# Optimization experiments

Hardware: AMD Instinct MI355X
Metric: run time of the kernel (lower is better)

## Reference

```python
import jax, jax.numpy as jnp
import numpy as np

N = 50000
E = 800000
NUM_KINDS = 100
D_NODE = 64
D_EDGE = 4
D_MSG = 64
L = 3
D_IN = 2 * D_NODE + D_EDGE  # 132


def setup_inputs() -> dict:
    key = jax.random.key(0)
    ks = jax.random.split(key, 20)

    def w(k, shape, fan_in):
        bound = 1.0 / np.sqrt(fan_in)
        return jax.random.uniform(k, shape, jnp.float32, -bound, bound)

    inp = {
        "edge_index": jax.random.randint(ks[0], (2, E), 0, N),
        "node_kind_ids": jax.random.randint(ks[1], (N,), 0, NUM_KINDS),
        "edge_attr": jax.random.normal(ks[2], (E, D_EDGE), jnp.float32),
        # learned params
        "emb": jax.random.normal(ks[3], (NUM_KINDS, D_NODE), jnp.float32),
        # stacked per-layer message MLP params [L, ...]
        "msg_w1": w(ks[4], (L, D_MSG, D_IN), D_IN),
        "msg_b1": w(ks[5], (L, D_MSG), D_IN),
        "msg_w2": w(ks[6], (L, D_MSG, D_MSG), D_MSG),
        "msg_b2": w(ks[7], (L, D_MSG), D_MSG),
        # stacked per-layer GRUCell params (torch layout: [3*d_node, d_in])
        "gru_wih": w(ks[8], (L, 3 * D_NODE, D_MSG), D_NODE),
        "gru_whh": w(ks[9], (L, 3 * D_NODE, D_NODE), D_NODE),
        "gru_bih": w(ks[10], (L, 3 * D_NODE), D_NODE),
        "gru_bhh": w(ks[11], (L, 3 * D_NODE), D_NODE),
        # edge head: Linear(132,64) -> SiLU -> Linear(64,1)
        "head_w1": w(ks[12], (64, D_IN), D_IN),
        "head_b1": w(ks[13], (64,), D_IN),
        "head_w2": w(ks[14], (1, 64), 64),
        "head_b2": w(ks[15], (1,), 64),
    }
    return inp


def reference(edge_index, node_kind_ids, edge_attr, emb,
              msg_w1, msg_b1, msg_w2, msg_b2,
              gru_wih, gru_whh, gru_bih, gru_bhh,
              head_w1, head_b1, head_w2, head_b2):
    src, dst = edge_index[0], edge_index[1]
    h = emb[node_kind_ids]  # [N, d_node]
    n_nodes = h.shape[0]
    for l in range(L):
        x = jnp.concatenate([h[src], h[dst], edge_attr], axis=1)  # [E, 132]
        m = jax.nn.silu(x @ msg_w1[l].T + msg_b1[l]) @ msg_w2[l].T + msg_b2[l]  # [E, d_msg]
        agg = jax.ops.segment_sum(m, dst, num_segments=n_nodes)  # [N, d_msg]
        # torch GRUCell math
        gi = agg @ gru_wih[l].T + gru_bih[l]  # [N, 3*d_node]
        gh = h @ gru_whh[l].T + gru_bhh[l]
        ir, iz, inn = jnp.split(gi, 3, axis=1)
        hr, hz, hn = jnp.split(gh, 3, axis=1)
        r = jax.nn.sigmoid(ir + hr)
        z = jax.nn.sigmoid(iz + hz)
        n = jnp.tanh(inn + r * hn)
        h = (1.0 - z) * n + z * h
    x = jnp.concatenate([h[src], h[dst], edge_attr], axis=1)  # [E, 132]
    logits = (jax.nn.silu(x @ head_w1.T + head_b1) @ head_w2.T + head_b2)[:, 0]
    return jax.nn.sigmoid(logits)  # [E]
```

## Files before the change

### kernel.cpp

```cpp
#include <hip/hip_runtime.h>
#include <hip/hip_bf16.h>


typedef __attribute__((ext_vector_type(8))) short bf16x8;
typedef __attribute__((ext_vector_type(4))) float f32x4;
#define MFMA16(a, b, c) __builtin_amdgcn_mfma_f32_16x16x32_bf16(a, b, c, 0, 0, 0)

#define CHUNK 128
#define XSTRIDE 272
#define MSTRIDE 264
#define HSTRIDE 144
#define SLABSZ 8704
#define HIDSZ  4608

#define WRZST 264
#define WNST  136

__device__ __forceinline__ float fast_sig(float x) { return 1.f / (1.f + __expf(-x)); }
__device__ __forceinline__ float fast_tanh(float x) {
    float ax = fabsf(x);
    float t = __expf(-2.f * ax);
    return copysignf((1.f - t) / (1.f + t), x);
}
__device__ __forceinline__ ushort f2bf(float f) {
    unsigned u = __float_as_uint(f);
    unsigned r = u + 0x7FFF + ((u >> 16) & 1);
    return (ushort)(r >> 16);
}

__global__ void prep_kernel(const float* __restrict__ msg_w1,
                            const float* __restrict__ msg_w2,
                            const float* __restrict__ gru_wih,
                            const float* __restrict__ gru_whh,
                            const float* __restrict__ head_w1,
                            const float* __restrict__ head_w2,
                            ushort* __restrict__ Wb1, ushort* __restrict__ Wb2,
                            ushort* __restrict__ Wh1, ushort* __restrict__ Wh2b,
                            ushort* __restrict__ Wrz, ushort* __restrict__ Wni,
                            ushort* __restrict__ Wnh) {
    int t = blockIdx.x * 256 + threadIdx.x;
    if (t < 30720) {
        int l = t / 10240, r = t % 10240, j = r / 160, k = r % 160;
        Wb1[t] = (k < 132) ? f2bf(msg_w1[l * 8448 + j * 132 + k]) : 0;
        return;
    }
    t -= 30720;
    if (t < 12288) {
        Wb2[t] = f2bf(msg_w2[t]);
        return;
    }
    t -= 12288;
    if (t < 10240) {
        int j = t / 160, k = t % 160;
        Wh1[t] = (k < 132) ? f2bf(head_w1[j * 132 + k]) : 0;
        return;
    }
    t -= 10240;
    if (t < 1024) {
        int j = t >> 6, k = t & 63;
        Wh2b[t] = (j == 0) ? f2bf(head_w2[k]) : 0;
        return;
    }
    t -= 1024;
    if (t < 49152) {
        int l = t / 16384, r = t % 16384, n = r >> 7, k = r & 127;
        float v = (k < 64) ? gru_wih[l * 12288 + n * 64 + k]
                           : gru_whh[l * 12288 + n * 64 + (k - 64)];
        Wrz[t] = f2bf(v);
        return;
    }
    t -= 49152;
    if (t < 12288) {
        int l = t / 4096, r = t % 4096, j = r >> 6, k = r & 63;
        Wni[t] = f2bf(gru_wih[l * 12288 + (128 + j) * 64 + k]);
        return;
    }
    t -= 12288;
    if (t < 12288) {
        int l = t / 4096, r = t % 4096, j = r >> 6, k = r & 63;
        Wnh[t] = f2bf(gru_whh[l * 12288 + (128 + j) * 64 + k]);
    }
}

__global__ void embed_kernel(float* __restrict__ h, ushort* __restrict__ hb,
                             const float* __restrict__ emb,
                             const int* __restrict__ kinds, int N) {
    int t = blockIdx.x * 256 + threadIdx.x;
    if (t >= N * 64) return;
    int node = t >> 6, d = t & 63;
    float v = emb[kinds[node] * 64 + d];
    h[t] = v;
    hb[t] = f2bf(v);
}

__global__ void hist_kernel(const int* __restrict__ dst, int* __restrict__ deg, int E) {
    int e = blockIdx.x * 256 + threadIdx.x;
    if (e < E) atomicAdd(&deg[dst[e]], 1);
}

__global__ void scan_kernel(const int* __restrict__ deg, int* __restrict__ cursor, int N) {
    __shared__ int sums[1024];
    int tid = threadIdx.x;
    int chunk = (N + 1023) >> 10;
    int lo = tid * chunk, hi = min(lo + chunk, N);
    int s = 0;
    for (int i = lo; i < hi; i++) s += deg[i];
    sums[tid] = s;
    __syncthreads();
    for (int off = 1; off < 1024; off <<= 1) {
        int v = (tid >= off) ? sums[tid - off] : 0;
        __syncthreads();
        sums[tid] += v;
        __syncthreads();
    }
    int run = (tid > 0) ? sums[tid - 1] : 0;
    for (int i = lo; i < hi; i++) {
        cursor[i] = run;
        run += deg[i];
    }
}

__global__ void scatter_kernel(const int* __restrict__ src, const int* __restrict__ dst,
                               const float* __restrict__ ea, int* __restrict__ cursor,
                               int* __restrict__ src_s, int* __restrict__ dst_s,
                               ushort* __restrict__ ea_sb, int E) {
    int e = blockIdx.x * 256 + threadIdx.x;
    if (e >= E) return;
    int d = dst[e];
    int p = atomicAdd(&cursor[d], 1);
    src_s[p] = src[e];
    dst_s[p] = d;
    float4 e4 = ((const float4*)ea)[e];
    ushort4 eb;
    eb.x = f2bf(e4.x); eb.y = f2bf(e4.y); eb.z = f2bf(e4.z); eb.w = f2bf(e4.w);
    ((ushort4*)ea_sb)[p] = eb;
}

__global__ __launch_bounds__(256) void edge_msg_mfma(
    const ushort* __restrict__ hb, const int* __restrict__ src_s,
    const int* __restrict__ dst_s, const ushort* __restrict__ ea_sb,
    const ushort* __restrict__ Wb1l, const ushort* __restrict__ Wb2l,
    const float* __restrict__ b1, const float* __restrict__ b2,
    float* __restrict__ agg, int E, int nchunks) {
    __shared__ char lds[4 * SLABSZ + 4 * HIDSZ];
    int tid = threadIdx.x;
    int w = tid >> 6, lane = tid & 63;
    int quad = lane >> 4, nrow = lane & 15;
    char* slab = lds + w * SLABSZ;
    char* hidb = lds + 4 * SLABSZ + w * HIDSZ;

    bf16x8 wf1[4][4], wfea[4], wf2[4][2];
    float b1v[4], b2v[4];
#pragma unroll
    for (int nt = 0; nt < 4; nt++) {
        int n = nt * 16 + nrow;
#pragma unroll
        for (int ks = 0; ks < 4; ks++)
            wf1[nt][ks] = *(const bf16x8*)(Wb1l + n * 160 + ks * 32 + quad * 8);
        wfea[nt] = *(const bf16x8*)(Wb1l + n * 160 + 128 + quad * 8);
#pragma unroll
        for (int ks = 0; ks < 2; ks++)
            wf2[nt][ks] = *(const bf16x8*)(Wb2l + n * 64 + ks * 32 + quad * 8);
        b1v[nt] = b1[n];
        b2v[nt] = b2[n];
    }

    for (int chunk = blockIdx.x; chunk < nchunks; chunk += gridDim.x) {
        int ebase = chunk * CHUNK;
        {
            int el = tid >> 1, half = tid & 1;
            int r = el & 31;
            int ec = min(ebase + el, E - 1);
            int node = half ? dst_s[ec] : src_s[ec];
            const float4* hrow = (const float4*)(hb + (size_t)node * 64);
            float4* xw = (float4*)(slab + r * XSTRIDE + half * 128);
#pragma unroll
            for (int i = 0; i < 8; i++) xw[i] = hrow[i];
        }
        bf16x8 ea0 = {0, 0, 0, 0, 0, 0, 0, 0};
        bf16x8 ea1 = {0, 0, 0, 0, 0, 0, 0, 0};
        if (quad == 0) {
            int ec0 = min(ebase + w * 32 + nrow, E - 1);
            int ec1 = min(ebase + w * 32 + 16 + nrow, E - 1);
            *(uint2*)&ea0 = *(const uint2*)(ea_sb + (size_t)ec0 * 4);
            *(uint2*)&ea1 = *(const uint2*)(ea_sb + (size_t)ec1 * 4);
        }
        f32x4 acc1[2][4];
#pragma unroll
        for (int mt = 0; mt < 2; mt++)
#pragma unroll
            for (int nt = 0; nt < 4; nt++) {
                f32x4 v;
                v[0] = v[1] = v[2] = v[3] = b1v[nt];
                acc1[mt][nt] = v;
            }
#pragma unroll
        for (int ks = 0; ks < 4; ks++) {
            bf16x8 a0 = *(const bf16x8*)(slab + nrow * XSTRIDE + ks * 64 + quad * 16);
            bf16x8 a1 = *(const bf16x8*)(slab + (16 + nrow) * XSTRIDE + ks * 64 + quad * 16);
#pragma unroll
            for (int nt = 0; nt < 4; nt++) {
                acc1[0][nt] = MFMA16(a0, wf1[nt][ks], acc1[0][nt]);
                acc1[1][nt] = MFMA16(a1, wf1[nt][ks], acc1[1][nt]);
            }
        }
#pragma unroll
        for (int nt = 0; nt < 4; nt++) {
            acc1[0][nt] = MFMA16(ea0, wfea[nt], acc1[0][nt]);
            acc1[1][nt] = MFMA16(ea1, wfea[nt], acc1[1][nt]);
        }
#pragma unroll
        for (int mt = 0; mt < 2; mt++)
#pragma unroll
            for (int nt = 0; nt < 4; nt++)
#pragma unroll
                for (int rg = 0; rg < 4; rg++) {
                    float v = acc1[mt][nt][rg];
                    v = v * fast_sig(v);
                    int rm = mt * 16 + quad * 4 + rg;
                    *(ushort*)(hidb + rm * HSTRIDE + (nt * 16 + nrow) * 2) = f2bf(v);
                }
        f32x4 acc2[2][4];
#pragma unroll
        for (int mt = 0; mt < 2; mt++)
#pragma unroll
            for (int nt = 0; nt < 4; nt++) {
                f32x4 v;
                v[0] = v[1] = v[2] = v[3] = b2v[nt];
                acc2[mt][nt] = v;
            }
#pragma unroll
        for (int ks = 0; ks < 2; ks++) {
            bf16x8 a0 = *(const bf16x8*)(hidb + nrow * HSTRIDE + ks * 64 + quad * 16);
            bf16x8 a1 = *(const bf16x8*)(hidb + (16 + nrow) * HSTRIDE + ks * 64 + quad * 16);
#pragma unroll
            for (int nt = 0; nt < 4; nt++) {
                acc2[0][nt] = MFMA16(a0, wf2[nt][ks], acc2[0][nt]);
                acc2[1][nt] = MFMA16(a1, wf2[nt][ks], acc2[1][nt]);
            }
        }
#pragma unroll
        for (int mt = 0; mt < 2; mt++)
#pragma unroll
            for (int nt = 0; nt < 4; nt++)
#pragma unroll
                for (int rg = 0; rg < 4; rg++) {
                    int rm = mt * 16 + quad * 4 + rg;
                    *(float*)(slab + rm * MSTRIDE + (nt * 16 + nrow) * 4) = acc2[mt][nt][rg];
                }
        {
            int e32 = ebase + w * 32;
            int dmy = dst_s[min(e32 + (lane & 31), E - 1)];
            int limit = min(32, E - e32);
            int nx = __shfl_down(dmy, 1);
            bool tl = ((lane & 31) == 31) || (dmy != nx);
            unsigned long long tm = __ballot(tl);
            float run = 0.f;
#pragma unroll
            for (int i = 0; i < 32; i++) {
                if (i < limit) {
                    run += *(const float*)(slab + i * MSTRIDE + lane * 4);
                    if (((tm >> i) & 1ull) || (i + 1 == limit)) {
                        int di = __shfl(dmy, i);
                        unsafeAtomicAdd(&agg[(size_t)di * 64 + lane], run);
                        run = 0.f;
                    }
                }
            }
        }
    }
}

__global__ __launch_bounds__(256) void head_mfma(
    const ushort* __restrict__ hb, const int* __restrict__ src,
    const int* __restrict__ dst, const float* __restrict__ ea,
    const ushort* __restrict__ Wh1, const ushort* __restrict__ Wh2b,
    const float* __restrict__ hb1, const float* __restrict__ hb2p,
    float* __restrict__ out, int E, int nchunks) {
    __shared__ char lds[4 * SLABSZ + 4 * HIDSZ];
    int tid = threadIdx.x;
    int w = tid >> 6, lane = tid & 63;
    int quad = lane >> 4, nrow = lane & 15;
    char* slab = lds + w * SLABSZ;
    char* hidb = lds + 4 * SLABSZ + w * HIDSZ;

    bf16x8 wf1[4][4], wfea[4], wh2[2];
    float b1v[4];
#pragma unroll
    for (int nt = 0; nt < 4; nt++) {
        int n = nt * 16 + nrow;
#pragma unroll
        for (int ks = 0; ks < 4; ks++)
            wf1[nt][ks] = *(const bf16x8*)(Wh1 + n * 160 + ks * 32 + quad * 8);
        wfea[nt] = *(const bf16x8*)(Wh1 + n * 160 + 128 + quad * 8);
        b1v[nt] = hb1[n];
    }
#pragma unroll
    for (int ks = 0; ks < 2; ks++)
        wh2[ks] = *(const bf16x8*)(Wh2b + nrow * 64 + ks * 32 + quad * 8);
    float hb2 = hb2p[0];

    for (int chunk = blockIdx.x; chunk < nchunks; chunk += gridDim.x) {
        int ebase = chunk * CHUNK;
        {
            int el = tid >> 1, half = tid & 1;
            int r = el & 31;
            int ec = min(ebase + el, E - 1);
            int node = half ? dst[ec] : src[ec];
            const float4* hrow = (const float4*)(hb + (size_t)node * 64);
            float4* xw = (float4*)(slab + r * XSTRIDE + half * 128);
#pragma unroll
            for (int i = 0; i < 8; i++) xw[i] = hrow[i];
        }
        bf16x8 ea0 = {0, 0, 0, 0, 0, 0, 0, 0};
        bf16x8 ea1 = {0, 0, 0, 0, 0, 0, 0, 0};
        if (quad == 0) {
            int ec0 = min(ebase + w * 32 + nrow, E - 1);
            int ec1 = min(ebase + w * 32 + 16 + nrow, E - 1);
            float4 e0 = ((const float4*)ea)[ec0];
            float4 e1 = ((const float4*)ea)[ec1];
            ushort4 u0, u1;
            u0.x = f2bf(e0.x); u0.y = f2bf(e0.y); u0.z = f2bf(e0.z); u0.w = f2bf(e0.w);
            u1.x = f2bf(e1.x); u1.y = f2bf(e1.y); u1.z = f2bf(e1.z); u1.w = f2bf(e1.w);
            *(ushort4*)&ea0 = u0;
            *(ushort4*)&ea1 = u1;
        }
        f32x4 acc1[2][4];
#pragma unroll
        for (int mt = 0; mt < 2; mt++)
#pragma unroll
            for (int nt = 0; nt < 4; nt++) {
                f32x4 v;
                v[0] = v[1] = v[2] = v[3] = b1v[nt];
                acc1[mt][nt] = v;
            }
#pragma unroll
        for (int ks = 0; ks < 4; ks++) {
            bf16x8 a0 = *(const bf16x8*)(slab + nrow * XSTRIDE + ks * 64 + quad * 16);
            bf16x8 a1 = *(const bf16x8*)(slab + (16 + nrow) * XSTRIDE + ks * 64 + quad * 16);
#pragma unroll
            for (int nt = 0; nt < 4; nt++) {
                acc1[0][nt] = MFMA16(a0, wf1[nt][ks], acc1[0][nt]);
                acc1[1][nt] = MFMA16(a1, wf1[nt][ks], acc1[1][nt]);
            }
        }
#pragma unroll
        for (int nt = 0; nt < 4; nt++) {
            acc1[0][nt] = MFMA16(ea0, wfea[nt], acc1[0][nt]);
            acc1[1][nt] = MFMA16(ea1, wfea[nt], acc1[1][nt]);
        }
#pragma unroll
        for (int mt = 0; mt < 2; mt++)
#pragma unroll
            for (int nt = 0; nt < 4; nt++)
#pragma unroll
                for (int rg = 0; rg < 4; rg++) {
                    float v = acc1[mt][nt][rg];
                    v = v * fast_sig(v);
                    int rm = mt * 16 + quad * 4 + rg;
                    *(ushort*)(hidb + rm * HSTRIDE + (nt * 16 + nrow) * 2) = f2bf(v);
                }
        f32x4 acc3[2];
#pragma unroll
        for (int mt = 0; mt < 2; mt++) {
            f32x4 v;
            v[0] = v[1] = v[2] = v[3] = 0.f;
            acc3[mt] = v;
        }
#pragma unroll
        for (int ks = 0; ks < 2; ks++) {
            bf16x8 a0 = *(const bf16x8*)(hidb + nrow * HSTRIDE + ks * 64 + quad * 16);
            bf16x8 a1 = *(const bf16x8*)(hidb + (16 + nrow) * HSTRIDE + ks * 64 + quad * 16);
            acc3[0] = MFMA16(a0, wh2[ks], acc3[0]);
            acc3[1] = MFMA16(a1, wh2[ks], acc3[1]);
        }
        if (nrow == 0) {
#pragma unroll
            for (int mt = 0; mt < 2; mt++)
#pragma unroll
                for (int rg = 0; rg < 4; rg++) {
                    int e = ebase + w * 32 + mt * 16 + quad * 4 + rg;
                    if (e < E) out[e] = fast_sig(acc3[mt][rg] + hb2);
                }
        }
    }
}

__device__ __forceinline__ bf16x8 aggfrag(const float* __restrict__ row, int off) {
    float4 f0 = *(const float4*)(row + off);
    float4 f1 = *(const float4*)(row + off + 4);
    bf16x8 r;
    r[0] = (short)f2bf(f0.x); r[1] = (short)f2bf(f0.y);
    r[2] = (short)f2bf(f0.z); r[3] = (short)f2bf(f0.w);
    r[4] = (short)f2bf(f1.x); r[5] = (short)f2bf(f1.y);
    r[6] = (short)f2bf(f1.z); r[7] = (short)f2bf(f1.w);
    return r;
}

__global__ __launch_bounds__(256) void gru_mfma(
    float* __restrict__ h, ushort* __restrict__ hb, float* __restrict__ agg,
    const ushort* __restrict__ Wrzg, const ushort* __restrict__ Wnig,
    const ushort* __restrict__ Wnhg,
    const float* __restrict__ bih, const float* __restrict__ bhh, int N) {
    __shared__ char lds[128 * WRZST + 2 * 64 * WNST];
    int tid = threadIdx.x, w = tid >> 6, lane = tid & 63;
    int quad = lane >> 4, nrow = lane & 15;
    char* wrz = lds;
    char* wni = lds + 128 * WRZST;
    char* wnh = wni + 64 * WNST;

    {
        int r = tid >> 1, half = tid & 1;
        const uint4* g = (const uint4*)(Wrzg + r * 128 + half * 64);
        uint4* d = (uint4*)(wrz + r * WRZST + half * 128);
#pragma unroll
        for (int i = 0; i < 8; i++) d[i] = g[i];
        if (tid < 128) {
            const uint4* g2 = (const uint4*)(Wnig + (tid >> 1) * 64 + (tid & 1) * 32);
            uint4* d2 = (uint4*)(wni + (tid >> 1) * WNST + (tid & 1) * 64);
#pragma unroll
            for (int i = 0; i < 4; i++) d2[i] = g2[i];
        } else {
            int t2 = tid - 128;
            const uint4* g2 = (const uint4*)(Wnhg + (t2 >> 1) * 64 + (t2 & 1) * 32);
            uint4* d2 = (uint4*)(wnh + (t2 >> 1) * WNST + (t2 & 1) * 64);
#pragma unroll
            for (int i = 0; i < 4; i++) d2[i] = g2[i];
        }
    }
    __syncthreads();

    int nb0 = blockIdx.x * 128 + w * 32;
    if (nb0 >= N) return;

    float brz[8], bi[4], bhv[4];
#pragma unroll
    for (int nt = 0; nt < 8; nt++) brz[nt] = bih[nt * 16 + nrow] + bhh[nt * 16 + nrow];
#pragma unroll
    for (int nt = 0; nt < 4; nt++) {
        bi[nt] = bih[128 + nt * 16 + nrow];
        bhv[nt] = bhh[128 + nt * 16 + nrow];
    }

    int n0 = min(nb0 + nrow, N - 1);
    int n1 = min(nb0 + 16 + nrow, N - 1);
    const float* ag0 = agg + (size_t)n0 * 64;
    const float* ag1 = agg + (size_t)n1 * 64;
    const ushort* hb0 = hb + (size_t)n0 * 64;
    const ushort* hb1 = hb + (size_t)n1 * 64;

    f32x4 accrz[2][8], acci[2][4], acch[2][4];
#pragma unroll
    for (int nt = 0; nt < 8; nt++) {
        f32x4 v; v[0] = v[1] = v[2] = v[3] = brz[nt];
        accrz[0][nt] = v; accrz[1][nt] = v;
    }
#pragma unroll
    for (int nt = 0; nt < 4; nt++) {
        f32x4 vi; vi[0] = vi[1] = vi[2] = vi[3] = bi[nt];
        acci[0][nt] = vi; acci[1][nt] = vi;
        f32x4 vh; vh[0] = vh[1] = vh[2] = vh[3] = bhv[nt];
        acch[0][nt] = vh; acch[1][nt] = vh;
    }

#pragma unroll
    for (int ks = 0; ks < 4; ks++) {
        bf16x8 a0, a1;
        if (ks < 2) {
            a0 = aggfrag(ag0, ks * 32 + quad * 8);
            a1 = aggfrag(ag1, ks * 32 + quad * 8);
        } else {
            a0 = *(const bf16x8*)(hb0 + (ks - 2) * 32 + quad * 8);
            a1 = *(const bf16x8*)(hb1 + (ks - 2) * 32 + quad * 8);
        }
#pragma unroll
        for (int nt = 0; nt < 8; nt++) {
            bf16x8 b = *(const bf16x8*)(wrz + (nt * 16 + nrow) * WRZST + ks * 64 + quad * 16);
            accrz[0][nt] = MFMA16(a0, b, accrz[0][nt]);
            accrz[1][nt] = MFMA16(a1, b, accrz[1][nt]);
        }
        if (ks < 2) {
#pragma unroll
            for (int nt = 0; nt < 4; nt++) {
                bf16x8 b = *(const bf16x8*)(wni + (nt * 16 + nrow) * WNST + ks * 64 + quad * 16);
                acci[0][nt] = MFMA16(a0, b, acci[0][nt]);
                acci[1][nt] = MFMA16(a1, b, acci[1][nt]);
            }
        } else {
#pragma unroll
            for (int nt = 0; nt < 4; nt++) {
                bf16x8 b = *(const bf16x8*)(wnh + (nt * 16 + nrow) * WNST + (ks - 2) * 64 + quad * 16);
                acch[0][nt] = MFMA16(a0, b, acch[0][nt]);
                acch[1][nt] = MFMA16(a1, b, acch[1][nt]);
            }
        }
    }

#pragma unroll
    for (int mt = 0; mt < 2; mt++)
#pragma unroll
        for (int nt = 0; nt < 4; nt++)
#pragma unroll
            for (int rg = 0; rg < 4; rg++) {
                int node = nb0 + mt * 16 + quad * 4 + rg;
                if (node < N) {
                    int col = nt * 16 + nrow;
                    float r = fast_sig(accrz[mt][nt][rg]);
                    float z = fast_sig(accrz[mt][nt + 4][rg]);
                    float nn = fast_tanh(acci[mt][nt][rg] + r * acch[mt][nt][rg]);
                    size_t idx = (size_t)node * 64 + col;
                    float ho = h[idx];
                    float hnew = (1.f - z) * nn + z * ho;
                    h[idx] = hnew;
                    hb[idx] = f2bf(hnew);
                }
            }

    {
        float4 z4 = {0.f, 0.f, 0.f, 0.f};
        if (nb0 + nrow < N) {
            float* a = agg + (size_t)(nb0 + nrow) * 64;
            *(float4*)(a + quad * 8) = z4;
            *(float4*)(a + quad * 8 + 4) = z4;
            *(float4*)(a + 32 + quad * 8) = z4;
            *(float4*)(a + 32 + quad * 8 + 4) = z4;
        }
        if (nb0 + 16 + nrow < N) {
            float* a = agg + (size_t)(nb0 + 16 + nrow) * 64;
            *(float4*)(a + quad * 8) = z4;
            *(float4*)(a + quad * 8 + 4) = z4;
            *(float4*)(a + 32 + quad * 8) = z4;
            *(float4*)(a + 32 + quad * 8 + 4) = z4;
        }
    }
}

extern "C" void kernel_launch(void* const* d_in, const int* in_sizes, int n_in,
                              void* d_out, int out_size, void* d_ws, size_t ws_size,
                              hipStream_t stream) {
    const int* edge_index = (const int*)d_in[0];
    int E = in_sizes[0] / 2;
    const int* src = edge_index;
    const int* dst = edge_index + E;
    const int* kinds = (const int*)d_in[1];
    int N = in_sizes[1];
    const float* edge_attr = (const float*)d_in[2];
    const float* emb = (const float*)d_in[3];
    const float* msg_w1 = (const float*)d_in[4];
    const float* msg_b1 = (const float*)d_in[5];
    const float* msg_w2 = (const float*)d_in[6];
    const float* msg_b2 = (const float*)d_in[7];
    const float* gru_wih = (const float*)d_in[8];
    const float* gru_whh = (const float*)d_in[9];
    const float* gru_bih = (const float*)d_in[10];
    const float* gru_bhh = (const float*)d_in[11];
    const float* head_w1 = (const float*)d_in[12];
    const float* head_b1 = (const float*)d_in[13];
    const float* head_w2 = (const float*)d_in[14];
    const float* head_b2 = (const float*)d_in[15];
    float* out = (float*)d_out;

    char* p = (char*)d_ws;
    float* h = (float*)p;        p += (size_t)N * 64 * 4;
    float* agg = (float*)p;      p += (size_t)N * 64 * 4;
    int* deg = (int*)p;          p += (size_t)N * 4;
    int* cursor = (int*)p;       p += (size_t)N * 4;
    int* src_s = (int*)p;        p += (size_t)E * 4;
    int* dst_s = (int*)p;        p += (size_t)E * 4;
    ushort* hb = (ushort*)p;     p += (size_t)N * 64 * 2;
    ushort* Wb1 = (ushort*)p;    p += 30720 * 2;
    ushort* Wb2 = (ushort*)p;    p += 12288 * 2;
    ushort* Wh1 = (ushort*)p;    p += 10240 * 2;
    ushort* Wh2b = (ushort*)p;   p += 1024 * 2;
    ushort* Wrz = (ushort*)p;    p += 49152 * 2;
    ushort* Wni = (ushort*)p;    p += 12288 * 2;
    ushort* Wnh = (ushort*)p;    p += 12288 * 2;
    ushort* ea_sb = (ushort*)p;  p += (size_t)E * 4 * 2;

    int nchunks = (E + CHUNK - 1) / CHUNK;

    prep_kernel<<<500, 256, 0, stream>>>(msg_w1, msg_w2, gru_wih, gru_whh, head_w1,
                                         head_w2, Wb1, Wb2, Wh1, Wh2b, Wrz, Wni, Wnh);
    embed_kernel<<<(N * 64 + 255) / 256, 256, 0, stream>>>(h, hb, emb, kinds, N);

    hipMemsetAsync(deg, 0, (size_t)N * sizeof(int), stream);
    hipMemsetAsync(agg, 0, (size_t)N * 64 * sizeof(float), stream);
    hist_kernel<<<(E + 255) / 256, 256, 0, stream>>>(dst, deg, E);
    scan_kernel<<<1, 1024, 0, stream>>>(deg, cursor, N);
    scatter_kernel<<<(E + 255) / 256, 256, 0, stream>>>(src, dst, edge_attr, cursor,
                                                        src_s, dst_s, ea_sb, E);

    for (int l = 0; l < 3; l++) {
        edge_msg_mfma<<<768, 256, 0, stream>>>(
            hb, src_s, dst_s, ea_sb,
            Wb1 + l * 10240, Wb2 + l * 4096,
            msg_b1 + l * 64, msg_b2 + l * 64, agg, E, nchunks);
        gru_mfma<<<(N + 127) / 128, 256, 0, stream>>>(
            h, hb, agg, Wrz + l * 16384, Wni + l * 4096, Wnh + l * 4096,
            gru_bih + l * 192, gru_bhh + l * 192, N);
    }
    head_mfma<<<768, 256, 0, stream>>>(hb, src, dst, edge_attr, Wh1, Wh2b,
                                       head_b1, head_b2, out, E, nchunks);
}
```

Before: 755.4 us.

## Halve edge chunk to 16 rows per wave and stage W2 in LDS

Each wave in the edge-message and head kernels now processes 16 edges per chunk instead of 32, which halves the accumulator and A-fragment registers. The second-layer message weights move from per-lane registers into a shared LDS copy loaded once per block. Together these lower register pressure and LDS footprint to raise occupancy and hide gather latency. In exchange there are more chunk iterations, extra LDS reads of W2 on every chunk, and less weight reuse per MFMA, plus shorter segment runs in the atomic aggregation, which may increase atomic count.

After: 885.0 us. 1.17x slower.

```diff
diff --git a/kernel.cpp b/kernel.cpp
--- a/kernel.cpp
+++ b/kernel.cpp
@@ -6,12 +6,14 @@
 typedef __attribute__((ext_vector_type(4))) float f32x4;
 #define MFMA16(a, b, c) __builtin_amdgcn_mfma_f32_16x16x32_bf16(a, b, c, 0, 0, 0)
 
-#define CHUNK 128
+#define CHUNK 64
 #define XSTRIDE 272
 #define MSTRIDE 264
 #define HSTRIDE 144
-#define SLABSZ 8704
-#define HIDSZ  4608
+#define SLABSZ 4352
+#define HIDSZ  2304
+#define WB2ST  136
+#define WB2SZ  8704
 
 #define WRZST 264
 #define WNST  136
@@ -142,14 +144,22 @@
     const ushort* __restrict__ Wb1l, const ushort* __restrict__ Wb2l,
     const float* __restrict__ b1, const float* __restrict__ b2,
     float* __restrict__ agg, int E, int nchunks) {
-    __shared__ char lds[4 * SLABSZ + 4 * HIDSZ];
+    __shared__ char lds[4 * SLABSZ + 4 * HIDSZ + WB2SZ];
     int tid = threadIdx.x;
     int w = tid >> 6, lane = tid & 63;
     int quad = lane >> 4, nrow = lane & 15;
     char* slab = lds + w * SLABSZ;
     char* hidb = lds + 4 * SLABSZ + w * HIDSZ;
-
-    bf16x8 wf1[4][4], wfea[4], wf2[4][2];
+    char* wb2 = lds + 4 * SLABSZ + 4 * HIDSZ;
+
+    {
+        int row = tid >> 2, q = tid & 3;
+        const uint4* g = (const uint4*)(Wb2l + row * 64 + q * 16);
+        uint4* d = (uint4*)(wb2 + row * WB2ST + q * 32);
+        d[0] = g[0];
+        d[1] = g[1];
+    }
+    bf16x8 wf1[4][4], wfea[4];
     float b1v[4], b2v[4];
 #pragma unroll
     for (int nt = 0; nt < 4; nt++) {
@@ -158,106 +168,86 @@
         for (int ks = 0; ks < 4; ks++)
             wf1[nt][ks] = *(const bf16x8*)(Wb1l + n * 160 + ks * 32 + quad * 8);
         wfea[nt] = *(const bf16x8*)(Wb1l + n * 160 + 128 + quad * 8);
-#pragma unroll
-        for (int ks = 0; ks < 2; ks++)
-            wf2[nt][ks] = *(const bf16x8*)(Wb2l + n * 64 + ks * 32 + quad * 8);
         b1v[nt] = b1[n];
         b2v[nt] = b2[n];
     }
+    __syncthreads();
 
     for (int chunk = blockIdx.x; chunk < nchunks; chunk += gridDim.x) {
         int ebase = chunk * CHUNK;
+        int e16 = ebase + w * 16;
         {
-            int el = tid >> 1, half = tid & 1;
-            int r = el & 31;
-            int ec = min(ebase + el, E - 1);
-            int node = half ? dst_s[ec] : src_s[ec];
-            const float4* hrow = (const float4*)(hb + (size_t)node * 64);
-            float4* xw = (float4*)(slab + r * XSTRIDE + half * 128);
-#pragma unroll
-            for (int i = 0; i < 8; i++) xw[i] = hrow[i];
+            int el = lane >> 2, part = lane & 3;
+            int ec = min(e16 + el, E - 1);
+            int node = (part < 2) ? src_s[ec] : dst_s[ec];
+            const float4* hrow = (const float4*)(hb + (size_t)node * 64 + (part & 1) * 32);
+            float4* xw = (float4*)(slab + el * XSTRIDE + part * 64);
+#pragma unroll
+            for (int i = 0; i < 4; i++) xw[i] = hrow[i];
         }
         bf16x8 ea0 = {0, 0, 0, 0, 0, 0, 0, 0};
-        bf16x8 ea1 = {0, 0, 0, 0, 0, 0, 0, 0};
         if (quad == 0) {
-            int ec0 = min(ebase + w * 32 + nrow, E - 1);
-            int ec1 = min(ebase + w * 32 + 16 + nrow, E - 1);
+            int ec0 = min(e16 + nrow, E - 1);
             *(uint2*)&ea0 = *(const uint2*)(ea_sb + (size_t)ec0 * 4);
-            *(uint2*)&ea1 = *(const uint2*)(ea_sb + (size_t)ec1 * 4);
-        }
-        f32x4 acc1[2][4];
-#pragma unroll
-        for (int mt = 0; mt < 2; mt++)
-#pragma unroll
-            for (int nt = 0; nt < 4; nt++) {
-                f32x4 v;
-                v[0] = v[1] = v[2] = v[3] = b1v[nt];
-                acc1[mt][nt] = v;
-            }
+        }
+        f32x4 acc1[4];
+#pragma unroll
+        for (int nt = 0; nt < 4; nt++) {
+            f32x4 v;
+            v[0] = v[1] = v[2] = v[3] = b1v[nt];
+            acc1[nt] = v;
+        }
 #pragma unroll
         for (int ks = 0; ks < 4; ks++) {
             bf16x8 a0 = *(const bf16x8*)(slab + nrow * XSTRIDE + ks * 64 + quad * 16);
-            bf16x8 a1 = *(const bf16x8*)(slab + (16 + nrow) * XSTRIDE + ks * 64 + quad * 16);
-#pragma unroll
-            for (int nt = 0; nt < 4; nt++) {
-                acc1[0][nt] = MFMA16(a0, wf1[nt][ks], acc1[0][nt]);
-                acc1[1][nt] = MFMA16(a1, wf1[nt][ks], acc1[1][nt]);
-            }
-        }
+#pragma unroll
+            for (int nt = 0; nt < 4; nt++)
+                acc1[nt] = MFMA16(a0, wf1[nt][ks], acc1[nt]);
+        }
+#pragma unroll
+        for (int nt = 0; nt < 4; nt++)
+            acc1[nt] = MFMA16(ea0, wfea[nt], acc1[nt]);
+#pragma unroll
+        for (int nt = 0; nt < 4; nt++)
+#pragma unroll
+            for (int rg = 0; rg < 4; rg++) {
+                float v = acc1[nt][rg];
+                v = v * fast_sig(v);
+                int rm = quad * 4 + rg;
+                *(ushort*)(hidb + rm * HSTRIDE + (nt * 16 + nrow) * 2) = f2bf(v);
+            }
+        f32x4 acc2[4];
 #pragma unroll
         for (int nt = 0; nt < 4; nt++) {
-            acc1[0][nt] = MFMA16(ea0, wfea[nt], acc1[0][nt]);
-            acc1[1][nt] = MFMA16(ea1, wfea[nt], acc1[1][nt]);
-        }
-#pragma unroll
-        for (int mt = 0; mt < 2; mt++)
-#pragma unroll
-            for (int nt = 0; nt < 4; nt++)
-#pragma unroll
-                for (int rg = 0; rg < 4; rg++) {
-                    float v = acc1[mt][nt][rg];
-                    v = v * fast_sig(v);
-                    int rm = mt * 16 + quad * 4 + rg;
-                    *(ushort*)(hidb + rm * HSTRIDE + (nt * 16 + nrow) * 2) = f2bf(v);
-                }
-        f32x4 acc2[2][4];
-#pragma unroll
-        for (int mt = 0; mt < 2; mt++)
-#pragma unroll
-            for (int nt = 0; nt < 4; nt++) {
-                f32x4 v;
-                v[0] = v[1] = v[2] = v[3] = b2v[nt];
-                acc2[mt][nt] = v;
-            }
+            f32x4 v;
+            v[0] = v[1] = v[2] = v[3] = b2v[nt];
+            acc2[nt] = v;
+        }
 #pragma unroll
         for (int ks = 0; ks < 2; ks++) {
             bf16x8 a0 = *(const bf16x8*)(hidb + nrow * HSTRIDE + ks * 64 + quad * 16);
-            bf16x8 a1 = *(const bf16x8*)(hidb + (16 + nrow) * HSTRIDE + ks * 64 + quad * 16);
 #pragma unroll
             for (int nt = 0; nt < 4; nt++) {
-                acc2[0][nt] = MFMA16(a0, wf2[nt][ks], acc2[0][nt]);
-                acc2[1][nt] = MFMA16(a1, wf2[nt][ks], acc2[1][nt]);
-            }
-        }
-#pragma unroll
-        for (int mt = 0; mt < 2; mt++)
-#pragma unroll
-            for (int nt = 0; nt < 4; nt++)
-#pragma unroll
-                for (int rg = 0; rg < 4; rg++) {
-                    int rm = mt * 16 + quad * 4 + rg;
-                    *(float*)(slab + rm * MSTRIDE + (nt * 16 + nrow) * 4) = acc2[mt][nt][rg];
-                }
+                bf16x8 b = *(const bf16x8*)(wb2 + (nt * 16 + nrow) * WB2ST + ks * 64 + quad * 16);
+                acc2[nt] = MFMA16(a0, b, acc2[nt]);
+            }
+        }
+#pragma unroll
+        for (int nt = 0; nt < 4; nt++)
+#pragma unroll
+            for (int rg = 0; rg < 4; rg++) {
+                int rm = quad * 4 + rg;
+                *(float*)(slab + rm * MSTRIDE + (nt * 16 + nrow) * 4) = acc2[nt][rg];
+            }
         {
-            int e32 = ebase + w * 32;
-            int dmy = dst_s[min(e32 + (lane & 31), E - 1)];
-            int limit = min(32, E - e32);
+            int dmy = dst_s[min(e16 + (lane & 15), E - 1)];
+            int limit = min(16, E - e16);
             int nx = __shfl_down(dmy, 1);
-            bool tl = ((lane & 31) == 31) || (dmy != nx);
+            bool tl = ((lane & 15) == 15) || (dmy != nx);
             unsigned long long tm = __ballot(tl);
             float run = 0.f;
 #pragma unroll
-            for (int i = 0; i < 32; i++) {
+            for (int i = 0; i < 16; i++) {
                 if (i < limit) {
                     run += *(const float*)(slab + i * MSTRIDE + lane * 4);
                     if (((tm >> i) & 1ull) || (i + 1 == limit)) {
@@ -302,86 +292,63 @@
 
     for (int chunk = blockIdx.x; chunk < nchunks; chunk += gridDim.x) {
         int ebase = chunk * CHUNK;
+        int e16 = ebase + w * 16;
         {
-            int el = tid >> 1, half = tid & 1;
-            int r = el & 31;
-            int ec = min(ebase + el, E - 1);
-            int node = half ? dst[ec] : src[ec];
-            const float4* hrow = (const float4*)(hb + (size_t)node * 64);
-            float4* xw = (float4*)(slab + r * XSTRIDE + half * 128);
-#pragma unroll
-            for (int i = 0; i < 8; i++) xw[i] = hrow[i];
+            int el = lane >> 2, part = lane & 3;
+            int ec = min(e16 + el, E - 1);
+            int node = (part < 2) ? src[ec] : dst[ec];
+            const float4* hrow = (const float4*)(hb + (size_t)node * 64 + (part & 1) * 32);
+            float4* xw = (float4*)(slab + el * XSTRIDE + part * 64);
+#pragma unroll
+            for (int i = 0; i < 4; i++) xw[i] = hrow[i];
         }
         bf16x8 ea0 = {0, 0, 0, 0, 0, 0, 0, 0};
-        bf16x8 ea1 = {0, 0, 0, 0, 0, 0, 0, 0};
         if (quad == 0) {
-            int ec0 = min(ebase + w * 32 + nrow, E - 1);
-            int ec1 = min(ebase + w * 32 + 16 + nrow, E - 1);
-            float4 e0 = ((const float4*)ea)[ec0];
-            float4 e1 = ((const float4*)ea)[ec1];
-            ushort4 u0, u1;
-            u0.x = f2bf(e0.x); u0.y = f2bf(e0.y); u0.z = f2bf(e0.z); u0.w = f2bf(e0.w);
-            u1.x = f2bf(e1.x); u1.y = f2bf(e1.y); u1.z = f2bf(e1.z); u1.w = f2bf(e1.w);
+            int ec0 = min(e16 + nrow, E - 1);
+            float4 e4 = ((const float4*)ea)[ec0];
+            ushort4 u0;
+            u0.x = f2bf(e4.x); u0.y = f2bf(e4.y); u0.z = f2bf(e4.z); u0.w = f2bf(e4.w);
             *(ushort4*)&ea0 = u0;
-            *(ushort4*)&ea1 = u1;
-        }
-        f32x4 acc1[2][4];
-#pragma unroll
-        for (int mt = 0; mt < 2; mt++)
-#pragma unroll
-            for (int nt = 0; nt < 4; nt++) {
-                f32x4 v;
-                v[0] = v[1] = v[2] = v[3] = b1v[nt];
-                acc1[mt][nt] = v;
-            }
+        }
+        f32x4 acc1[4];
+#pragma unroll
+        for (int nt = 0; nt < 4; nt++) {
+            f32x4 v;
+            v[0] = v[1] = v[2] = v[3] = b1v[nt];
+            acc1[nt] = v;
+        }
 #pragma unroll
         for (int ks = 0; ks < 4; ks++) {
             bf16x8 a0 = *(const bf16x8*)(slab + nrow * XSTRIDE + ks * 64 + quad * 16);
-            bf16x8 a1 = *(const bf16x8*)(slab + (16 + nrow) * XSTRIDE + ks * 64 + quad * 16);
-#pragma unroll
-            for (int nt = 0; nt < 4; nt++) {
-                acc1[0][nt] = MFMA16(a0, wf1[nt][ks], acc1[0][nt]);
-                acc1[1][nt] = MFMA16(a1, wf1[nt][ks], acc1[1][nt]);
-            }
-        }
-#pragma unroll
-        for (int nt = 0; nt < 4; nt++) {
-            acc1[0][nt] = MFMA16(ea0, wfea[nt], acc1[0][nt]);
-            acc1[1][nt] = MFMA16(ea1, wfea[nt], acc1[1][nt]);
-        }
-#pragma unroll
-        for (int mt = 0; mt < 2; mt++)
 #pragma unroll
             for (int nt = 0; nt < 4; nt++)
-#pragma unroll
-                for (int rg = 0; rg < 4; rg++) {
-                    float v = acc1[mt][nt][rg];
-                    v = v * fast_sig(v);
-                    int rm = mt * 16 + quad * 4 + rg;
-                    *(ushort*)(hidb + rm * HSTRIDE + (nt * 16 + nrow) * 2) = f2bf(v);
-                }
-        f32x4 acc3[2];
-#pragma unroll
-        for (int mt = 0; mt < 2; mt++) {
-            f32x4 v;
-            v[0] = v[1] = v[2] = v[3] = 0.f;
-            acc3[mt] = v;
-        }
+                acc1[nt] = MFMA16(a0, wf1[nt][ks], acc1[nt]);
+        }
+#pragma unroll
+        for (int nt = 0; nt < 4; nt++)
+            acc1[nt] = MFMA16(ea0, wfea[nt], acc1[nt]);
+#pragma unroll
+        for (int nt = 0; nt < 4; nt++)
+#pragma unroll
+            for (int rg = 0; rg < 4; rg++) {
+                float v = acc1[nt][rg];
+                v = v * fast_sig(v);
+                int rm = quad * 4 + rg;
+                *(ushort*)(hidb + rm * HSTRIDE + (nt * 16 + nrow) * 2) = f2bf(v);
+            }
+        f32x4 acc3;
+        acc3[0] = acc3[1] = acc3[2] = acc3[3] = 0.f;
 #pragma unroll
         for (int ks = 0; ks < 2; ks++) {
             bf16x8 a0 = *(const bf16x8*)(hidb + nrow * HSTRIDE + ks * 64 + quad * 16);
-            bf16x8 a1 = *(const bf16x8*)(hidb + (16 + nrow) * HSTRIDE + ks * 64 + quad * 16);
-            acc3[0] = MFMA16(a0, wh2[ks], acc3[0]);
-            acc3[1] = MFMA16(a1, wh2[ks], acc3[1]);
+            acc3 = MFMA16(a0, wh2[ks], acc3);
         }
         if (nrow == 0) {
 #pragma unroll
-            for (int mt = 0; mt < 2; mt++)
-#pragma unroll
-                for (int rg = 0; rg < 4; rg++) {
-                    int e = ebase + w * 32 + mt * 16 + quad * 4 + rg;
-                    if (e < E) out[e] = fast_sig(acc3[mt][rg] + hb2);
-                }
+            for (int rg = 0; rg < 4; rg++) {
+                int e = e16 + quad * 4 + rg;
+                if (e < E) out[e] = fast_sig(acc3[rg] + hb2);
+            }
         }
     }
 }
```

## Prefetch next chunk's gathered node rows into registers in edge kernels

Applied to the files above, without the earlier changes.

The edge message and head kernels now give each block a contiguous range of chunks instead of a grid-stride range. While the current chunk is computed, the gathered h rows for the next chunk are loaded into registers, hiding gather latency behind the MFMA work. The grid shrinks from 768 to 512 blocks so each block handles more chunks in sequence. The prefetch buffer adds register pressure that could lower occupancy, and with fewer blocks there is less parallelism to hide latency. Because rows are now indexed by w*32+r rather than by tid, each wave gathers its own rows.

Result: slower. 793.4 us (+5.0%).

```diff
diff --git a/kernel.cpp b/kernel.cpp
--- a/kernel.cpp
+++ b/kernel.cpp
@@ -165,17 +165,35 @@
         b2v[nt] = b2[n];
     }
 
-    for (int chunk = blockIdx.x; chunk < nchunks; chunk += gridDim.x) {
+    int per = (nchunks + gridDim.x - 1) / gridDim.x;
+    int c0 = blockIdx.x * per;
+    int c1 = min(c0 + per, nchunks);
+    if (c0 >= c1) return;
+
+    int r = lane >> 1, half = lane & 1;
+
+    float4 pf[8];
+    {
+        int ec = min(c0 * CHUNK + w * 32 + r, E - 1);
+        int node = half ? dst_s[ec] : src_s[ec];
+        const float4* hrow = (const float4*)(hb + (size_t)node * 64);
+#pragma unroll
+        for (int i = 0; i < 8; i++) pf[i] = hrow[i];
+    }
+
+    for (int chunk = c0; chunk < c1; chunk++) {
         int ebase = chunk * CHUNK;
         {
-            int el = tid >> 1, half = tid & 1;
-            int r = el & 31;
-            int ec = min(ebase + el, E - 1);
+            float4* xw = (float4*)(slab + r * XSTRIDE + half * 128);
+#pragma unroll
+            for (int i = 0; i < 8; i++) xw[i] = pf[i];
+        }
+        if (chunk + 1 < c1) {
+            int ec = min((chunk + 1) * CHUNK + w * 32 + r, E - 1);
             int node = half ? dst_s[ec] : src_s[ec];
             const float4* hrow = (const float4*)(hb + (size_t)node * 64);
-            float4* xw = (float4*)(slab + r * XSTRIDE + half * 128);
-#pragma unroll
-            for (int i = 0; i < 8; i++) xw[i] = hrow[i];
+#pragma unroll
+            for (int i = 0; i < 8; i++) pf[i] = hrow[i];
         }
         bf16x8 ea0 = {0, 0, 0, 0, 0, 0, 0, 0};
         bf16x8 ea1 = {0, 0, 0, 0, 0, 0, 0, 0};
@@ -300,17 +318,34 @@
         wh2[ks] = *(const bf16x8*)(Wh2b + nrow * 64 + ks * 32 + quad * 8);
     float hb2 = hb2p[0];
 
-    for (int chunk = blockIdx.x; chunk < nchunks; chunk += gridDim.x) {
+    int per = (nchunks + gridDim.x - 1) / gridDim.x;
+    int c0 = blockIdx.x * per;
+    int c1 = min(c0 + per, nchunks);
+    if (c0 >= c1) return;
+
+    int r = lane >> 1, half = lane & 1;
+    float4 pf[8];
+    {
+        int ec = min(c0 * CHUNK + w * 32 + r, E - 1);
+        int node = half ? dst[ec] : src[ec];
+        const float4* hrow = (const float4*)(hb + (size_t)node * 64);
+#pragma unroll
+        for (int i = 0; i < 8; i++) pf[i] = hrow[i];
+    }
+
+    for (int chunk = c0; chunk < c1; chunk++) {
         int ebase = chunk * CHUNK;
         {
-            int el = tid >> 1, half = tid & 1;
-            int r = el & 31;
-            int ec = min(ebase + el, E - 1);
+            float4* xw = (float4*)(slab + r * XSTRIDE + half * 128);
+#pragma unroll
+            for (int i = 0; i < 8; i++) xw[i] = pf[i];
+        }
+        if (chunk + 1 < c1) {
+            int ec = min((chunk + 1) * CHUNK + w * 32 + r, E - 1);
             int node = half ? dst[ec] : src[ec];
             const float4* hrow = (const float4*)(hb + (size_t)node * 64);
-            float4* xw = (float4*)(slab + r * XSTRIDE + half * 128);
-#pragma unroll
-            for (int i = 0; i < 8; i++) xw[i] = hrow[i];
+#pragma unroll
+            for (int i = 0; i < 8; i++) pf[i] = hrow[i];
         }
         bf16x8 ea0 = {0, 0, 0, 0, 0, 0, 0, 0};
         bf16x8 ea1 = {0, 0, 0, 0, 0, 0, 0, 0};
@@ -591,7 +626,7 @@
                                                         src_s, dst_s, ea_sb, E);
 
     for (int l = 0; l < 3; l++) {
-        edge_msg_mfma<<<768, 256, 0, stream>>>(
+        edge_msg_mfma<<<512, 256, 0, stream>>>(
             hb, src_s, dst_s, ea_sb,
             Wb1 + l * 10240, Wb2 + l * 4096,
             msg_b1 + l * 64, msg_b2 + l * 64, agg, E, nchunks);
@@ -599,6 +634,6 @@
             h, hb, agg, Wrz + l * 16384, Wni + l * 4096, Wnh + l * 4096,
             gru_bih + l * 192, gru_bhh + l * 192, N);
     }
-    head_mfma<<<768, 256, 0, stream>>>(hb, src, dst, edge_attr, Wh1, Wh2b,
+    head_mfma<<<512, 256, 0, stream>>>(hb, src, dst, edge_attr, Wh1, Wh2b,
                                        head_b1, head_b2, out, E, nchunks);
 }
```

## Gather node features directly into MFMA fragments and move weights to LDS

Applied to the files above, without the earlier changes.

The edge message and head kernels now load src/dst node rows from global memory straight into MFMA A-operand registers. The LDS staging slab they replace is dropped, and the hidden buffer now reuses the per-wave slab. The second-layer and edge-attr weight fragments move from registers into shared LDS to cut VGPR pressure and LDS footprint, which may raise occupancy. Chunks are assigned as contiguous ranges per block instead of grid-strided, which improves dst locality for the segmented atomic reduction. In exchange, each MFMA step now issues extra LDS weight reads, and the global gathers are less coalesced (16-byte pieces per lane).

After: 914.7 us. 1.21x slower.

```diff
diff --git a/kernel.cpp b/kernel.cpp
--- a/kernel.cpp
+++ b/kernel.cpp
@@ -7,11 +7,15 @@
 #define MFMA16(a, b, c) __builtin_amdgcn_mfma_f32_16x16x32_bf16(a, b, c, 0, 0, 0)
 
 #define CHUNK 128
-#define XSTRIDE 272
 #define MSTRIDE 264
 #define HSTRIDE 144
-#define SLABSZ 8704
-#define HIDSZ  4608
+#define SLABSZ 8448
+#define WB2ST 136
+#define WB2SZ 8704
+#define WEAST 80
+#define WEASZ 5120
+
+#define HHSLAB 4608
 
 #define WRZST 264
 #define WNST  136
@@ -142,14 +146,21 @@
     const ushort* __restrict__ Wb1l, const ushort* __restrict__ Wb2l,
     const float* __restrict__ b1, const float* __restrict__ b2,
     float* __restrict__ agg, int E, int nchunks) {
-    __shared__ char lds[4 * SLABSZ + 4 * HIDSZ];
+    __shared__ char lds[4 * SLABSZ + WB2SZ + WEASZ];
     int tid = threadIdx.x;
     int w = tid >> 6, lane = tid & 63;
     int quad = lane >> 4, nrow = lane & 15;
     char* slab = lds + w * SLABSZ;
-    char* hidb = lds + 4 * SLABSZ + w * HIDSZ;
-
-    bf16x8 wf1[4][4], wfea[4], wf2[4][2];
+    char* wb2 = lds + 4 * SLABSZ;
+    char* wea = wb2 + WB2SZ;
+
+    {
+        int row = tid >> 2, q = tid & 3;
+        *(uint4*)(wb2 + row * WB2ST + q * 32) = *(const uint4*)(Wb2l + row * 64 + q * 16);
+        *(uint4*)(wb2 + row * WB2ST + q * 32 + 16) = *(const uint4*)(Wb2l + row * 64 + q * 16 + 8);
+        *(uint4*)(wea + row * WEAST + q * 16) = *(const uint4*)(Wb1l + row * 160 + 128 + q * 8);
+    }
+    bf16x8 wf1[4][4];
     float b1v[4], b2v[4];
 #pragma unroll
     for (int nt = 0; nt < 4; nt++) {
@@ -157,33 +168,36 @@
 #pragma unroll
         for (int ks = 0; ks < 4; ks++)
             wf1[nt][ks] = *(const bf16x8*)(Wb1l + n * 160 + ks * 32 + quad * 8);
-        wfea[nt] = *(const bf16x8*)(Wb1l + n * 160 + 128 + quad * 8);
-#pragma unroll
-        for (int ks = 0; ks < 2; ks++)
-            wf2[nt][ks] = *(const bf16x8*)(Wb2l + n * 64 + ks * 32 + quad * 8);
         b1v[nt] = b1[n];
         b2v[nt] = b2[n];
     }
-
-    for (int chunk = blockIdx.x; chunk < nchunks; chunk += gridDim.x) {
+    __syncthreads();
+
+    int per = (nchunks + gridDim.x - 1) / gridDim.x;
+    int c0 = blockIdx.x * per;
+    int c1 = min(c0 + per, nchunks);
+    if (c0 >= c1) return;
+
+    for (int chunk = c0; chunk < c1; chunk++) {
         int ebase = chunk * CHUNK;
-        {
-            int el = tid >> 1, half = tid & 1;
-            int r = el & 31;
-            int ec = min(ebase + el, E - 1);
-            int node = half ? dst_s[ec] : src_s[ec];
-            const float4* hrow = (const float4*)(hb + (size_t)node * 64);
-            float4* xw = (float4*)(slab + r * XSTRIDE + half * 128);
-#pragma unroll
-            for (int i = 0; i < 8; i++) xw[i] = hrow[i];
-        }
+        int e0 = min(ebase + w * 32 + nrow, E - 1);
+        int e1 = min(ebase + w * 32 + 16 + nrow, E - 1);
+        int s0 = src_s[e0], d0 = dst_s[e0];
+        int s1 = src_s[e1], d1 = dst_s[e1];
+        bf16x8 a0[4], a1[4];
+        a0[0] = *(const bf16x8*)(hb + (size_t)s0 * 64 + quad * 8);
+        a0[1] = *(const bf16x8*)(hb + (size_t)s0 * 64 + 32 + quad * 8);
+        a0[2] = *(const bf16x8*)(hb + (size_t)d0 * 64 + quad * 8);
+        a0[3] = *(const bf16x8*)(hb + (size_t)d0 * 64 + 32 + quad * 8);
+        a1[0] = *(const bf16x8*)(hb + (size_t)s1 * 64 + quad * 8);
+        a1[1] = *(const bf16x8*)(hb + (size_t)s1 * 64 + 32 + quad * 8);
+        a1[2] = *(const bf16x8*)(hb + (size_t)d1 * 64 + quad * 8);
+        a1[3] = *(const bf16x8*)(hb + (size_t)d1 * 64 + 32 + quad * 8);
         bf16x8 ea0 = {0, 0, 0, 0, 0, 0, 0, 0};
         bf16x8 ea1 = {0, 0, 0, 0, 0, 0, 0, 0};
         if (quad == 0) {
-            int ec0 = min(ebase + w * 32 + nrow, E - 1);
-            int ec1 = min(ebase + w * 32 + 16 + nrow, E - 1);
-            *(uint2*)&ea0 = *(const uint2*)(ea_sb + (size_t)ec0 * 4);
-            *(uint2*)&ea1 = *(const uint2*)(ea_sb + (size_t)ec1 * 4);
+            *(uint2*)&ea0 = *(const uint2*)(ea_sb + (size_t)e0 * 4);
+            *(uint2*)&ea1 = *(const uint2*)(ea_sb + (size_t)e1 * 4);
         }
         f32x4 acc1[2][4];
 #pragma unroll
@@ -196,18 +210,17 @@
             }
 #pragma unroll
         for (int ks = 0; ks < 4; ks++) {
-            bf16x8 a0 = *(const bf16x8*)(slab + nrow * XSTRIDE + ks * 64 + quad * 16);
-            bf16x8 a1 = *(const bf16x8*)(slab + (16 + nrow) * XSTRIDE + ks * 64 + quad * 16);
-#pragma unroll
-            for (int nt = 0; nt < 4; nt++) {
-                acc1[0][nt] = MFMA16(a0, wf1[nt][ks], acc1[0][nt]);
-                acc1[1][nt] = MFMA16(a1, wf1[nt][ks], acc1[1][nt]);
+#pragma unroll
+            for (int nt = 0; nt < 4; nt++) {
+                acc1[0][nt] = MFMA16(a0[ks], wf1[nt][ks], acc1[0][nt]);
+                acc1[1][nt] = MFMA16(a1[ks], wf1[nt][ks], acc1[1][nt]);
             }
         }
 #pragma unroll
         for (int nt = 0; nt < 4; nt++) {
-            acc1[0][nt] = MFMA16(ea0, wfea[nt], acc1[0][nt]);
-            acc1[1][nt] = MFMA16(ea1, wfea[nt], acc1[1][nt]);
+            bf16x8 wf = *(const bf16x8*)(wea + (nt * 16 + nrow) * WEAST + quad * 16);
+            acc1[0][nt] = MFMA16(ea0, wf, acc1[0][nt]);
+            acc1[1][nt] = MFMA16(ea1, wf, acc1[1][nt]);
         }
 #pragma unroll
         for (int mt = 0; mt < 2; mt++)
@@ -218,7 +231,7 @@
                     float v = acc1[mt][nt][rg];
                     v = v * fast_sig(v);
                     int rm = mt * 16 + quad * 4 + rg;
-                    *(ushort*)(hidb + rm * HSTRIDE + (nt * 16 + nrow) * 2) = f2bf(v);
+                    *(ushort*)(slab + rm * HSTRIDE + (nt * 16 + nrow) * 2) = f2bf(v);
                 }
         f32x4 acc2[2][4];
 #pragma unroll
@@ -231,12 +244,13 @@
             }
 #pragma unroll
         for (int ks = 0; ks < 2; ks++) {
-            bf16x8 a0 = *(const bf16x8*)(hidb + nrow * HSTRIDE + ks * 64 + quad * 16);
-            bf16x8 a1 = *(const bf16x8*)(hidb + (16 + nrow) * HSTRIDE + ks * 64 + quad * 16);
-#pragma unroll
-            for (int nt = 0; nt < 4; nt++) {
-                acc2[0][nt] = MFMA16(a0, wf2[nt][ks], acc2[0][nt]);
-                acc2[1][nt] = MFMA16(a1, wf2[nt][ks], acc2[1][nt]);
+            bf16x8 h0 = *(const bf16x8*)(slab + nrow * HSTRIDE + ks * 64 + quad * 16);
+            bf16x8 h1 = *(const bf16x8*)(slab + (16 + nrow) * HSTRIDE + ks * 64 + quad * 16);
+#pragma unroll
+            for (int nt = 0; nt < 4; nt++) {
+                bf16x8 b = *(const bf16x8*)(wb2 + (nt * 16 + nrow) * WB2ST + ks * 64 + quad * 16);
+                acc2[0][nt] = MFMA16(h0, b, acc2[0][nt]);
+                acc2[1][nt] = MFMA16(h1, b, acc2[1][nt]);
             }
         }
 #pragma unroll
@@ -277,14 +291,18 @@
     const ushort* __restrict__ Wh1, const ushort* __restrict__ Wh2b,
     const float* __restrict__ hb1, const float* __restrict__ hb2p,
     float* __restrict__ out, int E, int nchunks) {
-    __shared__ char lds[4 * SLABSZ + 4 * HIDSZ];
+    __shared__ char lds[4 * HHSLAB + WEASZ];
     int tid = threadIdx.x;
     int w = tid >> 6, lane = tid & 63;
     int quad = lane >> 4, nrow = lane & 15;
-    char* slab = lds + w * SLABSZ;
-    char* hidb = lds + 4 * SLABSZ + w * HIDSZ;
-
-    bf16x8 wf1[4][4], wfea[4], wh2[2];
+    char* hidb = lds + w * HHSLAB;
+    char* wea = lds + 4 * HHSLAB;
+
+    {
+        int row = tid >> 2, q = tid & 3;
+        *(uint4*)(wea + row * WEAST + q * 16) = *(const uint4*)(Wh1 + row * 160 + 128 + q * 8);
+    }
+    bf16x8 wf1[4][4], wh2[2];
     float b1v[4];
 #pragma unroll
     for (int nt = 0; nt < 4; nt++) {
@@ -292,36 +310,42 @@
 #pragma unroll
         for (int ks = 0; ks < 4; ks++)
             wf1[nt][ks] = *(const bf16x8*)(Wh1 + n * 160 + ks * 32 + quad * 8);
-        wfea[nt] = *(const bf16x8*)(Wh1 + n * 160 + 128 + quad * 8);
         b1v[nt] = hb1[n];
     }
 #pragma unroll
     for (int ks = 0; ks < 2; ks++)
         wh2[ks] = *(const bf16x8*)(Wh2b + nrow * 64 + ks * 32 + quad * 8);
     float hb2 = hb2p[0];
-
-    for (int chunk = blockIdx.x; chunk < nchunks; chunk += gridDim.x) {
+    __syncthreads();
+
+    int per = (nchunks + gridDim.x - 1) / gridDim.x;
+    int c0 = blockIdx.x * per;
+    int c1 = min(c0 + per, nchunks);
+    if (c0 >= c1) return;
+
+    for (int chunk = c0; chunk < c1; chunk++) {
         int ebase = chunk * CHUNK;
-        {
-            int el = tid >> 1, half = tid & 1;
-            int r = el & 31;
-            int ec = min(ebase + el, E - 1);
-            int node = half ? dst[ec] : src[ec];
-            const float4* hrow = (const float4*)(hb + (size_t)node * 64);
-            float4* xw = (float4*)(slab + r * XSTRIDE + half * 128);
-#pragma unroll
-            for (int i = 0; i < 8; i++) xw[i] = hrow[i];
-        }
+        int e0 = min(ebase + w * 32 + nrow, E - 1);
+        int e1 = min(ebase + w * 32 + 16 + nrow, E - 1);
+        int s0 = src[e0], d0 = dst[e0];
+        int s1 = src[e1], d1 = dst[e1];
+        bf16x8 a0[4], a1[4];
+        a0[0] = *(const bf16x8*)(hb + (size_t)s0 * 64 + quad * 8);
+        a0[1] = *(const bf16x8*)(hb + (size_t)s0 * 64 + 32 + quad * 8);
+        a0[2] = *(const bf16x8*)(hb + (size_t)d0 * 64 + quad * 8);
+        a0[3] = *(const bf16x8*)(hb + (size_t)d0 * 64 + 32 + quad * 8);
+        a1[0] = *(const bf16x8*)(hb + (size_t)s1 * 64 + quad * 8);
+        a1[1] = *(const bf16x8*)(hb + (size_t)s1 * 64 + 32 + quad * 8);
+        a1[2] = *(const bf16x8*)(hb + (size_t)d1 * 64 + quad * 8);
+        a1[3] = *(const bf16x8*)(hb + (size_t)d1 * 64 + 32 + quad * 8);
         bf16x8 ea0 = {0, 0, 0, 0, 0, 0, 0, 0};
         bf16x8 ea1 = {0, 0, 0, 0, 0, 0, 0, 0};
         if (quad == 0) {
-            int ec0 = min(ebase + w * 32 + nrow, E - 1);
-            int ec1 = min(ebase + w * 32 + 16 + nrow, E - 1);
-            float4 e0 = ((const float4*)ea)[ec0];
-            float4 e1 = ((const float4*)ea)[ec1];
+            float4 f0 = ((const float4*)ea)[e0];
+            float4 f1 = ((const float4*)ea)[e1];
             ushort4 u0, u1;
-            u0.x = f2bf(e0.x); u0.y = f2bf(e0.y); u0.z = f2bf(e0.z); u0.w = f2bf(e0.w);
-            u1.x = f2bf(e1.x); u1.y = f2bf(e1.y); u1.z = f2bf(e1.z); u1.w = f2bf(e1.w);
+            u0.x = f2bf(f0.x); u0.y = f2bf(f0.y); u0.z = f2bf(f0.z); u0.w = f2bf(f0.w);
+            u1.x = f2bf(f1.x); u1.y = f2bf(f1.y); u1.z = f2bf(f1.z); u1.w = f2bf(f1.w);
             *(ushort4*)&ea0 = u0;
             *(ushort4*)&ea1 = u1;
         }
@@ -336,18 +360,17 @@
             }
 #pragma unroll
         for (int ks = 0; ks < 4; ks++) {
-            bf16x8 a0 = *(const bf16x8*)(slab + nrow * XSTRIDE + ks * 64 + quad * 16);
-            bf16x8 a1 = *(const bf16x8*)(slab + (16 + nrow) * XSTRIDE + ks * 64 + quad * 16);
-#pragma unroll
-            for (int nt = 0; nt < 4; nt++) {
-                acc1[0][nt] = MFMA16(a0, wf1[nt][ks], acc1[0][nt]);
-                acc1[1][nt] = MFMA16(a1, wf1[nt][ks], acc1[1][nt]);
+#pragma unroll
+            for (int nt = 0; nt < 4; nt++) {
+                acc1[0][nt] = MFMA16(a0[ks], wf1[nt][ks], acc1[0][nt]);
+                acc1[1][nt] = MFMA16(a1[ks], wf1[nt][ks], acc1[1][nt]);
             }
         }
 #pragma unroll
         for (int nt = 0; nt < 4; nt++) {
-            acc1[0][nt] = MFMA16(ea0, wfea[nt], acc1[0][nt]);
-            acc1[1][nt] = MFMA16(ea1, wfea[nt], acc1[1][nt]);
+            bf16x8 wf = *(const bf16x8*)(wea + (nt * 16 + nrow) * WEAST + quad * 16);
+            acc1[0][nt] = MFMA16(ea0, wf, acc1[0][nt]);
+            acc1[1][nt] = MFMA16(ea1, wf, acc1[1][nt]);
         }
 #pragma unroll
         for (int mt = 0; mt < 2; mt++)
@@ -369,10 +392,10 @@
         }
 #pragma unroll
         for (int ks = 0; ks < 2; ks++) {
-            bf16x8 a0 = *(const bf16x8*)(hidb + nrow * HSTRIDE + ks * 64 + quad * 16);
-            bf16x8 a1 = *(const bf16x8*)(hidb + (16 + nrow) * HSTRIDE + ks * 64 + quad * 16);
-            acc3[0] = MFMA16(a0, wh2[ks], acc3[0]);
-            acc3[1] = MFMA16(a1, wh2[ks], acc3[1]);
+            bf16x8 h0 = *(const bf16x8*)(hidb + nrow * HSTRIDE + ks * 64 + quad * 16);
+            bf16x8 h1 = *(const bf16x8*)(hidb + (16 + nrow) * HSTRIDE + ks * 64 + quad * 16);
+            acc3[0] = MFMA16(h0, wh2[ks], acc3[0]);
+            acc3[1] = MFMA16(h1, wh2[ks], acc3[1]);
         }
         if (nrow == 0) {
 #pragma unroll
```
